# Kernel optimization log

Hardware: AMD Instinct MI355X
Metric: run time of the kernel (lower is better)

The kernel has to match this reference:

```python
import jax, jax.numpy as jnp
import numpy as np

EMBED_DIM = 1024
NUM_HEADS = 16
HEAD_DIM = EMBED_DIM // NUM_HEADS
NEG_INF = -1e9


def setup_inputs() -> dict:
    key = jax.random.key(0)
    k1, k2, k3, k4, k5 = jax.random.split(key, 5)
    # ragged batch: 8 segments, alternating lengths 1024 / 512 -> 6144 tokens
    lengths = np.array([1024, 512, 1024, 512, 1024, 512, 1024, 512], dtype=np.int32)
    cu_seqlens = np.concatenate([[0], np.cumsum(lengths)]).astype(np.int32)
    total = int(cu_seqlens[-1])  # 6144
    scale = 0.02
    return {
        "hidden_states": jax.random.normal(k1, (total, EMBED_DIM), dtype=jnp.float32),
        "proj_weight": jax.random.normal(k2, (3 * EMBED_DIM, EMBED_DIM), dtype=jnp.float32) * scale,
        "proj_bias": jax.random.normal(k3, (3 * EMBED_DIM,), dtype=jnp.float32) * scale,
        "out_weight": jax.random.normal(k4, (EMBED_DIM, EMBED_DIM), dtype=jnp.float32) * scale,
        "out_bias": jax.random.normal(k5, (EMBED_DIM,), dtype=jnp.float32) * scale,
        "cu_seqlens": jnp.asarray(cu_seqlens),
        "max_len": 1024,
    }


def reference(hidden_states, proj_weight, proj_bias, out_weight, out_bias, cu_seqlens, max_len):
    T = hidden_states.shape[0]
    B = cu_seqlens.shape[0] - 1
    H, Dh = NUM_HEADS, HEAD_DIM
    softmax_scale = 1.0 / jnp.sqrt(jnp.float32(Dh))

    # fused QKV projection: [T, 3E] -> [T, H, 3, Dh]
    qkv = hidden_states @ proj_weight.T + proj_bias
    qkv = qkv.reshape(T, H, 3, Dh)
    q, k, v = qkv[:, :, 0], qkv[:, :, 1], qkv[:, :, 2]  # each [T, H, Dh]

    # unpack ragged tokens into padded [B, S, H, Dh]
    lengths = cu_seqlens[1:] - cu_seqlens[:-1]            # [B]
    pos = jnp.arange(max_len)                              # [S]
    valid = pos[None, :] < lengths[:, None]                # [B, S]
    idx = jnp.where(valid, cu_seqlens[:-1, None] + pos[None, :], 0)  # [B, S]
    qp, kp, vp = q[idx], k[idx], v[idx]                    # [B, S, H, Dh]

    # per-segment attention (non-causal encoder self-attn)
    scores = jnp.einsum("bqhd,bkhd->bhqk", qp, kp) * softmax_scale  # [B,H,S,S]
    scores = jnp.where(valid[:, None, None, :], scores, NEG_INF)
    probs = jax.nn.softmax(scores, axis=-1)
    ctx = jnp.einsum("bhqk,bkhd->bqhd", probs, vp)         # [B, S, H, Dh]

    # pack back to ragged [T, E]; invalid slots scattered out-of-bounds (dropped)
    scatter_idx = jnp.where(valid, idx, T).reshape(-1)     # [B*S]
    ctx_flat = ctx.reshape(B * max_len, H * Dh)
    context = jnp.zeros((T, H * Dh), dtype=ctx_flat.dtype).at[scatter_idx].set(
        ctx_flat, mode="drop")

    return context @ out_weight.T + out_bias
```

## Files before the change

kernel.cpp:

```cpp
#include <hip/hip_runtime.h>
#include <math.h>

#define EMBED 1024
#define NHEAD 16
#define HDIM 64
#define QKV_LD 3072
#define SM_SCALE_LOG2 0.18033688f

typedef _Float16 f16x8 __attribute__((ext_vector_type(8)));
typedef float f32x4 __attribute__((ext_vector_type(4)));
typedef unsigned short ushort8v __attribute__((ext_vector_type(8)));
typedef unsigned short ushort4v __attribute__((ext_vector_type(4)));

__device__ __forceinline__ void gload16(const void* g, void* l) {
    __builtin_amdgcn_global_load_lds(
        (const __attribute__((address_space(1))) unsigned int*)g,
        (__attribute__((address_space(3))) unsigned int*)l, 16, 0, 0);
}

__device__ __forceinline__ int xcd_swz(int bid, int nwg) {
    int cpx = nwg >> 3;
    return (bid & 7) * cpx + (bid >> 3);
}

__device__ __forceinline__ int swz(int row, int col) {
    return row * 72 + (col ^ (((row >> 3) & 7) << 3));
}

__global__ __launch_bounds__(256) void cvt3_f32_f16(
    const float* __restrict__ xa, _Float16* __restrict__ ya, int nA,
    const float* __restrict__ xb, _Float16* __restrict__ yb, int nB,
    const float* __restrict__ xc, _Float16* __restrict__ yc, int nC)
{
    int i = blockIdx.x * 256 + threadIdx.x;
    const float* x;
    _Float16* y;
    if (i < nA)               { x = xa; y = ya; }
    else if (i < nA + nB)     { x = xb; y = yb; i -= nA; }
    else if (i < nA + nB + nC){ x = xc; y = yc; i -= nA + nB; }
    else return;
    float4 v = reinterpret_cast<const float4*>(x)[i];
    unsigned short h0 = __builtin_bit_cast(unsigned short, (_Float16)v.x);
    unsigned short h1 = __builtin_bit_cast(unsigned short, (_Float16)v.y);
    unsigned short h2 = __builtin_bit_cast(unsigned short, (_Float16)v.z);
    unsigned short h3 = __builtin_bit_cast(unsigned short, (_Float16)v.w);
    reinterpret_cast<ushort4*>(y)[i] = make_ushort4(h0, h1, h2, h3);
}

template <bool F16_OUT>
__global__ __launch_bounds__(256) void gemm_m97(
    const _Float16* __restrict__ A, const _Float16* __restrict__ B,
    const float* __restrict__ bias, float* __restrict__ Cf,
    _Float16* __restrict__ Ch, int M, int N, int K, int gx)
{
    __shared__ __align__(16) unsigned short sA[128 * 64];
    __shared__ __align__(16) unsigned short sB[128 * 64];

    const int nwg = gridDim.x;
    const int wgid = xcd_swz(blockIdx.x, nwg);
    const int row0 = (wgid / gx) * 128;
    const int col0 = (wgid % gx) * 128;

    const int tid = threadIdx.x;
    const int lane = tid & 63;
    const int w = tid >> 6;
    const int wr = w >> 1;
    const int wc = w & 1;
    const int c = lane & 15;
    const int g = lane >> 4;

    const unsigned short* Au = (const unsigned short*)A;
    const unsigned short* Bu = (const unsigned short*)B;

    f32x4 acc[4][4];
    #pragma unroll
    for (int m = 0; m < 4; m++)
        #pragma unroll
        for (int n = 0; n < 4; n++)
            acc[m][n] = (f32x4){0.f, 0.f, 0.f, 0.f};

    size_t aoff[4], boff[4];
    int ldst[4];
    #pragma unroll
    for (int i = 0; i < 4; i++) {
        int chunk = (i * 4 + w) * 64 + lane;
        int row = chunk >> 3;
        int scol = ((chunk & 7) ^ (row & 7)) * 8;
        aoff[i] = (size_t)min(row0 + row, M - 1) * K + scol;
        boff[i] = (size_t)min(col0 + row, N - 1) * K + scol;
        ldst[i] = chunk * 8;
    }

    for (int k0 = 0; k0 < K; k0 += 64) {
        __syncthreads();
        #pragma unroll
        for (int i = 0; i < 4; i++) {
            gload16(Au + aoff[i] + k0, &sA[ldst[i]]);
            gload16(Bu + boff[i] + k0, &sB[ldst[i]]);
        }
        __syncthreads();

        #pragma unroll
        for (int ks = 0; ks < 2; ks++) {
            f16x8 af[4], bf[4];
            #pragma unroll
            for (int m = 0; m < 4; m++) {
                int row = wr * 64 + m * 16 + c;
                int cc = (ks * 4 + g) ^ (row & 7);
                af[m] = __builtin_bit_cast(f16x8, *reinterpret_cast<const ushort8v*>(
                            &sA[row * 64 + cc * 8]));
            }
            #pragma unroll
            for (int n = 0; n < 4; n++) {
                int row = wc * 64 + n * 16 + c;
                int cc = (ks * 4 + g) ^ (row & 7);
                bf[n] = __builtin_bit_cast(f16x8, *reinterpret_cast<const ushort8v*>(
                            &sB[row * 64 + cc * 8]));
            }
            #pragma unroll
            for (int m = 0; m < 4; m++)
                #pragma unroll
                for (int n = 0; n < 4; n++)
                    acc[m][n] = __builtin_amdgcn_mfma_f32_16x16x32_f16(af[m], bf[n], acc[m][n], 0, 0, 0);
        }
    }

    #pragma unroll
    for (int m = 0; m < 4; m++) {
        #pragma unroll
        for (int n = 0; n < 4; n++) {
            int cc = col0 + wc * 64 + n * 16 + c;
            if (cc >= N) continue;
            float bv = bias[cc];
            #pragma unroll
            for (int j = 0; j < 4; j++) {
                int r = row0 + wr * 64 + m * 16 + g * 4 + j;
                if (r >= M) continue;
                float v = acc[m][n][j] + bv;
                if constexpr (F16_OUT) {
                    Ch[(size_t)r * N + cc] = (_Float16)v;
                } else {
                    Cf[(size_t)r * N + cc] = v;
                }
            }
        }
    }
}

__global__ __launch_bounds__(256) void attn_mfma(
    const _Float16* __restrict__ qkv, const int* __restrict__ cu,
    _Float16* __restrict__ ctx, int B, int maxTiles)
{
    __shared__ __align__(16) unsigned short sK[64 * 72];
    __shared__ __align__(16) unsigned short sV[64 * 72];

    const int nwg = gridDim.x;
    const int wgid = xcd_swz(blockIdx.x, nwg);
    const int h = wgid / maxTiles;
    const int tile = wgid % maxTiles;

    int b = -1, q0 = 0, accum = 0;
    for (int i = 0; i < B; i++) {
        int len = cu[i + 1] - cu[i];
        int nt = (len + 63) >> 6;
        if (tile < accum + nt) { b = i; q0 = (tile - accum) << 6; break; }
        accum += nt;
    }
    if (b < 0) return;
    const int s0 = cu[b];
    const int L = cu[b + 1] - s0;
    if (q0 >= L) return;

    const int tid = threadIdx.x;
    const int lane = tid & 63;
    const int w = tid >> 6;
    const int g = lane >> 4;
    const int c = lane & 15;
    const size_t qcol = (size_t)h * 192;
    const unsigned short* qkvu = (const unsigned short*)qkv;

    f16x8 q[2];
    {
        int qrow = min(q0 + w * 16 + c, L - 1);
        size_t off = (size_t)(s0 + qrow) * QKV_LD + qcol + g * 8;
        q[0] = *reinterpret_cast<const f16x8*>(&qkv[off]);
        q[1] = *reinterpret_cast<const f16x8*>(&qkv[off + 32]);
    }

    f32x4 o[4];
    #pragma unroll
    for (int n = 0; n < 4; n++) o[n] = (f32x4){0.f, 0.f, 0.f, 0.f};
    float m_r = -INFINITY;
    float l_r = 0.f;

    for (int kc = 0; kc < L; kc += 64) {
        __syncthreads();
        #pragma unroll
        for (int it = 0; it < 2; it++) {
            int idx = it * 256 + tid;
            int r = idx >> 3;
            int d0 = (idx & 7) * 8;
            int gr = min(kc + r, L - 1);
            size_t off = (size_t)(s0 + gr) * QKV_LD + qcol + 64 + d0;
            *reinterpret_cast<uint4*>(&sK[swz(r, d0)]) =
                *reinterpret_cast<const uint4*>(&qkvu[off]);
            ushort8v vv = *reinterpret_cast<const ushort8v*>(&qkvu[off + 64]);
            #pragma unroll
            for (int j = 0; j < 8; j++)
                sV[swz(d0 + j, r)] = vv[j];
        }
        __syncthreads();

        __builtin_amdgcn_s_setprio(1);
        f32x4 sacc[4];
        #pragma unroll
        for (int f = 0; f < 4; f++) sacc[f] = (f32x4){0.f, 0.f, 0.f, 0.f};
        #pragma unroll
        for (int f = 0; f < 4; f++) {
            #pragma unroll
            for (int ks = 0; ks < 2; ks++) {
                f16x8 kf = __builtin_bit_cast(f16x8, *reinterpret_cast<const ushort8v*>(
                               &sK[swz(f * 16 + c, ks * 32 + g * 8)]));
                sacc[f] = __builtin_amdgcn_mfma_f32_16x16x32_f16(kf, q[ks], sacc[f], 0, 0, 0);
            }
        }
        __builtin_amdgcn_s_setprio(0);

        float mx = -INFINITY;
        if (kc + 64 <= L) {
            #pragma unroll
            for (int f = 0; f < 4; f++) {
                #pragma unroll
                for (int j = 0; j < 4; j++) {
                    float v = sacc[f][j] * SM_SCALE_LOG2;
                    sacc[f][j] = v;
                    mx = fmaxf(mx, v);
                }
            }
        } else {
            #pragma unroll
            for (int f = 0; f < 4; f++) {
                #pragma unroll
                for (int j = 0; j < 4; j++) {
                    float v = sacc[f][j] * SM_SCALE_LOG2;
                    if (kc + f * 16 + g * 4 + j >= L) v = -1.0e9f;
                    sacc[f][j] = v;
                    mx = fmaxf(mx, v);
                }
            }
        }
        mx = fmaxf(mx, __shfl_xor(mx, 16));
        mx = fmaxf(mx, __shfl_xor(mx, 32));

        const bool nskip = !__all(mx - m_r <= 8.0f);
        const float mn = nskip ? fmaxf(m_r, mx) : m_r;

        unsigned int paw[4][2];
        float rs = 0.f;
        #pragma unroll
        for (int f = 0; f < 4; f++) {
            float p0 = exp2f(sacc[f][0] - mn);
            float p1 = exp2f(sacc[f][1] - mn);
            float p2 = exp2f(sacc[f][2] - mn);
            float p3 = exp2f(sacc[f][3] - mn);
            rs += (p0 + p1) + (p2 + p3);
            unsigned int h0 = __builtin_bit_cast(unsigned short, (_Float16)p0);
            unsigned int h1 = __builtin_bit_cast(unsigned short, (_Float16)p1);
            unsigned int h2 = __builtin_bit_cast(unsigned short, (_Float16)p2);
            unsigned int h3 = __builtin_bit_cast(unsigned short, (_Float16)p3);
            paw[f][0] = h0 | (h1 << 16);
            paw[f][1] = h2 | (h3 << 16);
        }
        rs += __shfl_xor(rs, 16);
        rs += __shfl_xor(rs, 32);

        if (nskip) {
            float fs = exp2f(m_r - mn);
            l_r = l_r * fs + rs;
            m_r = mn;
            #pragma unroll
            for (int j = 0; j < 4; j++) {
                float fq = __shfl(fs, (lane & 48) | (g * 4 + j));
                #pragma unroll
                for (int n = 0; n < 4; n++)
                    o[n][j] *= fq;
            }
        } else {
            l_r += rs;
        }

        __builtin_amdgcn_s_setprio(1);
        #pragma unroll
        for (int ks = 0; ks < 2; ks++) {
            uint4 pw;
            pw.x = paw[2 * ks][0];
            pw.y = paw[2 * ks][1];
            pw.z = paw[2 * ks + 1][0];
            pw.w = paw[2 * ks + 1][1];
            f16x8 pa = __builtin_bit_cast(f16x8, pw);
            #pragma unroll
            for (int n = 0; n < 4; n++) {
                uint2 lo = *reinterpret_cast<const uint2*>(
                               &sV[swz(n * 16 + c, ks * 32 + g * 4)]);
                uint2 hi = *reinterpret_cast<const uint2*>(
                               &sV[swz(n * 16 + c, ks * 32 + 16 + g * 4)]);
                uint4 vw;
                vw.x = lo.x; vw.y = lo.y; vw.z = hi.x; vw.w = hi.y;
                f16x8 vf = __builtin_bit_cast(f16x8, vw);
                o[n] = __builtin_amdgcn_mfma_f32_16x16x32_f16(pa, vf, o[n], 0, 0, 0);
            }
        }
        __builtin_amdgcn_s_setprio(0);
    }

    float linv[4];
    {
        float il = 1.0f / l_r;
        #pragma unroll
        for (int j = 0; j < 4; j++)
            linv[j] = __shfl(il, (lane & 48) | (g * 4 + j));
    }
    #pragma unroll
    for (int n = 0; n < 4; n++) {
        #pragma unroll
        for (int j = 0; j < 4; j++) {
            int r = q0 + w * 16 + g * 4 + j;
            if (r >= L) continue;
            ctx[(size_t)(s0 + r) * EMBED + h * HDIM + n * 16 + c] =
                (_Float16)(o[n][j] * linv[j]);
        }
    }
}

extern "C" void kernel_launch(void* const* d_in, const int* in_sizes, int n_in,
                              void* d_out, int out_size, void* d_ws, size_t ws_size,
                              hipStream_t stream) {
    const float* hs = (const float*)d_in[0];
    const float* pw = (const float*)d_in[1];
    const float* pb = (const float*)d_in[2];
    const float* ow = (const float*)d_in[3];
    const float* ob = (const float*)d_in[4];
    const int*   cu = (const int*)d_in[5];

    const int T = in_sizes[0] / EMBED;
    const int B = in_sizes[5] - 1;

    char* p = (char*)d_ws;
    size_t hsF_b  = (size_t)T * EMBED * sizeof(_Float16);
    size_t pwF_b  = (size_t)3 * EMBED * EMBED * sizeof(_Float16);
    size_t owF_b  = (size_t)EMBED * EMBED * sizeof(_Float16);
    size_t qkvF_b = (size_t)T * QKV_LD * sizeof(_Float16);
    size_t ctxF_b = hsF_b;

    _Float16* hsF  = (_Float16*)p;  p += hsF_b;
    _Float16* pwF  = (_Float16*)p;  p += pwF_b;
    _Float16* owF  = (_Float16*)p;  p += owF_b;
    _Float16* qkvF = (_Float16*)p;  p += qkvF_b;
    _Float16* ctxF = (_Float16*)p;  p += ctxF_b;

    float* out = (float*)d_out;
    dim3 blk(256);

    {
        int nA = T * EMBED / 4;
        int nB = 3 * EMBED * EMBED / 4;
        int nC = EMBED * EMBED / 4;
        int total = nA + nB + nC;
        cvt3_f32_f16<<<(total + 255) / 256, blk, 0, stream>>>(
            hs, hsF, nA, pw, pwF, nB, ow, owF, nC);
    }

    {
        int gx = (3 * EMBED) / 128;
        int nwg = gx * ((T + 127) / 128);
        gemm_m97<true><<<nwg, blk, 0, stream>>>(hsF, pwF, pb,
                                                (float*)nullptr, qkvF,
                                                T, 3 * EMBED, EMBED, gx);
    }

    {
        int maxTiles = T / 64 + B;
        int nwg = NHEAD * maxTiles;
        attn_mfma<<<nwg, blk, 0, stream>>>(qkvF, cu, ctxF, B, maxTiles);
    }

    {
        int gx = EMBED / 128;
        int nwg = gx * ((T + 127) / 128);
        gemm_m97<false><<<nwg, blk, 0, stream>>>(ctxF, owF, ob,
                                                 out, (_Float16*)nullptr,
                                                 T, EMBED, EMBED, gx);
    }
}
```

Measured before the change: 174.1 us.

## Load K fragments directly from global and register-prefetch next V tile

Drops the shared-memory staging buffer for K. Each wave now reads its own K MFMA fragments straight from global memory into registers. The V tile for the next iteration is prefetched into registers while the current one is consumed, so its global latency overlaps the compute. The aim is to cut LDS traffic and to hide V load latency. In exchange, each of the four waves reloads the same K rows from global or L2 (four times the K reads), and register pressure goes up.

Result: slower. 217.9 us (+25.2%).

```diff
diff --git a/kernel.cpp b/kernel.cpp
--- a/kernel.cpp
+++ b/kernel.cpp
@@ -151,7 +151,6 @@
     const _Float16* __restrict__ qkv, const int* __restrict__ cu,
     _Float16* __restrict__ ctx, int B, int maxTiles)
 {
-    __shared__ __align__(16) unsigned short sK[64 * 72];
     __shared__ __align__(16) unsigned short sV[64 * 72];
 
     const int nwg = gridDim.x;
@@ -187,6 +186,19 @@
         q[1] = *reinterpret_cast<const f16x8*>(&qkv[off + 32]);
     }
 
+    const int r0_ = tid >> 3;
+    const int r1_ = 32 + r0_;
+    const int d0_ = (tid & 7) * 8;
+    const size_t vband = qcol + 128 + d0_;
+
+    ushort8v vv0, vv1;
+    {
+        int gr0 = min(r0_, L - 1);
+        int gr1 = min(r1_, L - 1);
+        vv0 = *reinterpret_cast<const ushort8v*>(&qkvu[(size_t)(s0 + gr0) * QKV_LD + vband]);
+        vv1 = *reinterpret_cast<const ushort8v*>(&qkvu[(size_t)(s0 + gr1) * QKV_LD + vband]);
+    }
+
     f32x4 o[4];
     #pragma unroll
     for (int n = 0; n < 4; n++) o[n] = (f32x4){0.f, 0.f, 0.f, 0.f};
@@ -194,20 +206,29 @@
     float l_r = 0.f;
 
     for (int kc = 0; kc < L; kc += 64) {
+        f16x8 kf[4][2];
+        #pragma unroll
+        for (int f = 0; f < 4; f++) {
+            int kr = min(kc + f * 16 + c, L - 1);
+            size_t koff = (size_t)(s0 + kr) * QKV_LD + qcol + 64 + g * 8;
+            kf[f][0] = *reinterpret_cast<const f16x8*>(&qkv[koff]);
+            kf[f][1] = *reinterpret_cast<const f16x8*>(&qkv[koff + 32]);
+        }
+
         __syncthreads();
         #pragma unroll
-        for (int it = 0; it < 2; it++) {
-            int idx = it * 256 + tid;
-            int r = idx >> 3;
-            int d0 = (idx & 7) * 8;
-            int gr = min(kc + r, L - 1);
-            size_t off = (size_t)(s0 + gr) * QKV_LD + qcol + 64 + d0;
-            *reinterpret_cast<uint4*>(&sK[swz(r, d0)]) =
-                *reinterpret_cast<const uint4*>(&qkvu[off]);
-            ushort8v vv = *reinterpret_cast<const ushort8v*>(&qkvu[off + 64]);
-            #pragma unroll
-            for (int j = 0; j < 8; j++)
-                sV[swz(d0 + j, r)] = vv[j];
+        for (int j = 0; j < 8; j++)
+            sV[swz(d0_ + j, r0_)] = vv0[j];
+        #pragma unroll
+        for (int j = 0; j < 8; j++)
+            sV[swz(d0_ + j, r1_)] = vv1[j];
+
+        if (kc + 64 < L) {
+            int nkc = kc + 64;
+            int gr0 = min(nkc + r0_, L - 1);
+            int gr1 = min(nkc + r1_, L - 1);
+            vv0 = *reinterpret_cast<const ushort8v*>(&qkvu[(size_t)(s0 + gr0) * QKV_LD + vband]);
+            vv1 = *reinterpret_cast<const ushort8v*>(&qkvu[(size_t)(s0 + gr1) * QKV_LD + vband]);
         }
         __syncthreads();
 
@@ -218,11 +239,8 @@
         #pragma unroll
         for (int f = 0; f < 4; f++) {
             #pragma unroll
-            for (int ks = 0; ks < 2; ks++) {
-                f16x8 kf = __builtin_bit_cast(f16x8, *reinterpret_cast<const ushort8v*>(
-                               &sK[swz(f * 16 + c, ks * 32 + g * 8)]));
-                sacc[f] = __builtin_amdgcn_mfma_f32_16x16x32_f16(kf, q[ks], sacc[f], 0, 0, 0);
-            }
+            for (int ks = 0; ks < 2; ks++)
+                sacc[f] = __builtin_amdgcn_mfma_f32_16x16x32_f16(kf[f][ks], q[ks], sacc[f], 0, 0, 0);
         }
         __builtin_amdgcn_s_setprio(0);
 
```

## Double-buffer K/V tiles in attention with register prefetch of next chunk

Applied to the files above, without the earlier changes.

The attention kernel now keeps two LDS buffers for K and V. The next 64-row chunk is loaded from global memory into registers before the current chunk's QK and PV MFMAs, then written to the alternate buffer afterwards. This hides global load latency behind compute and cuts the barriers per iteration from two to one. In exchange it doubles LDS use and raises register pressure, which can lower occupancy.

Result: slower. 178.6 us (+2.6%).

```diff
diff --git a/kernel.cpp b/kernel.cpp
--- a/kernel.cpp
+++ b/kernel.cpp
@@ -151,8 +151,8 @@
     const _Float16* __restrict__ qkv, const int* __restrict__ cu,
     _Float16* __restrict__ ctx, int B, int maxTiles)
 {
-    __shared__ __align__(16) unsigned short sK[64 * 72];
-    __shared__ __align__(16) unsigned short sV[64 * 72];
+    __shared__ __align__(16) unsigned short sK[2][64 * 72];
+    __shared__ __align__(16) unsigned short sV[2][64 * 72];
 
     const int nwg = gridDim.x;
     const int wgid = xcd_swz(blockIdx.x, nwg);
@@ -187,6 +187,34 @@
         q[1] = *reinterpret_cast<const f16x8*>(&qkv[off + 32]);
     }
 
+    const int r0_ = tid >> 3;
+    const int r1_ = 32 + r0_;
+    const int d0_ = (tid & 7) * 8;
+    const int lk0 = swz(r0_, d0_);
+    const int lk1 = swz(r1_, d0_);
+    const size_t kband = qcol + 64 + d0_;
+    const size_t vband = qcol + 128 + d0_;
+
+    uint4 kr0, kr1;
+    ushort8v vv0, vv1;
+
+    {
+        int g0 = min(r0_, L - 1);
+        int g1 = min(r1_, L - 1);
+        kr0 = *reinterpret_cast<const uint4*>(&qkvu[(size_t)(s0 + g0) * QKV_LD + kband]);
+        kr1 = *reinterpret_cast<const uint4*>(&qkvu[(size_t)(s0 + g1) * QKV_LD + kband]);
+        vv0 = *reinterpret_cast<const ushort8v*>(&qkvu[(size_t)(s0 + g0) * QKV_LD + vband]);
+        vv1 = *reinterpret_cast<const ushort8v*>(&qkvu[(size_t)(s0 + g1) * QKV_LD + vband]);
+        *reinterpret_cast<uint4*>(&sK[0][lk0]) = kr0;
+        *reinterpret_cast<uint4*>(&sK[0][lk1]) = kr1;
+        #pragma unroll
+        for (int j = 0; j < 8; j++) {
+            sV[0][swz(d0_ + j, r0_)] = vv0[j];
+            sV[0][swz(d0_ + j, r1_)] = vv1[j];
+        }
+    }
+    __syncthreads();
+
     f32x4 o[4];
     #pragma unroll
     for (int n = 0; n < 4; n++) o[n] = (f32x4){0.f, 0.f, 0.f, 0.f};
@@ -194,22 +222,18 @@
     float l_r = 0.f;
 
     for (int kc = 0; kc < L; kc += 64) {
-        __syncthreads();
-        #pragma unroll
-        for (int it = 0; it < 2; it++) {
-            int idx = it * 256 + tid;
-            int r = idx >> 3;
-            int d0 = (idx & 7) * 8;
-            int gr = min(kc + r, L - 1);
-            size_t off = (size_t)(s0 + gr) * QKV_LD + qcol + 64 + d0;
-            *reinterpret_cast<uint4*>(&sK[swz(r, d0)]) =
-                *reinterpret_cast<const uint4*>(&qkvu[off]);
-            ushort8v vv = *reinterpret_cast<const ushort8v*>(&qkvu[off + 64]);
-            #pragma unroll
-            for (int j = 0; j < 8; j++)
-                sV[swz(d0 + j, r)] = vv[j];
-        }
-        __syncthreads();
+        const int p = (kc >> 6) & 1;
+        const bool more = (kc + 64 < L);
+
+        if (more) {
+            int nk = kc + 64;
+            int g0 = min(nk + r0_, L - 1);
+            int g1 = min(nk + r1_, L - 1);
+            kr0 = *reinterpret_cast<const uint4*>(&qkvu[(size_t)(s0 + g0) * QKV_LD + kband]);
+            kr1 = *reinterpret_cast<const uint4*>(&qkvu[(size_t)(s0 + g1) * QKV_LD + kband]);
+            vv0 = *reinterpret_cast<const ushort8v*>(&qkvu[(size_t)(s0 + g0) * QKV_LD + vband]);
+            vv1 = *reinterpret_cast<const ushort8v*>(&qkvu[(size_t)(s0 + g1) * QKV_LD + vband]);
+        }
 
         __builtin_amdgcn_s_setprio(1);
         f32x4 sacc[4];
@@ -220,7 +244,7 @@
             #pragma unroll
             for (int ks = 0; ks < 2; ks++) {
                 f16x8 kf = __builtin_bit_cast(f16x8, *reinterpret_cast<const ushort8v*>(
-                               &sK[swz(f * 16 + c, ks * 32 + g * 8)]));
+                               &sK[p][swz(f * 16 + c, ks * 32 + g * 8)]));
                 sacc[f] = __builtin_amdgcn_mfma_f32_16x16x32_f16(kf, q[ks], sacc[f], 0, 0, 0);
             }
         }
@@ -301,9 +325,9 @@
             #pragma unroll
             for (int n = 0; n < 4; n++) {
                 uint2 lo = *reinterpret_cast<const uint2*>(
-                               &sV[swz(n * 16 + c, ks * 32 + g * 4)]);
+                               &sV[p][swz(n * 16 + c, ks * 32 + g * 4)]);
                 uint2 hi = *reinterpret_cast<const uint2*>(
-                               &sV[swz(n * 16 + c, ks * 32 + 16 + g * 4)]);
+                               &sV[p][swz(n * 16 + c, ks * 32 + 16 + g * 4)]);
                 uint4 vw;
                 vw.x = lo.x; vw.y = lo.y; vw.z = hi.x; vw.w = hi.y;
                 f16x8 vf = __builtin_bit_cast(f16x8, vw);
@@ -311,6 +335,17 @@
             }
         }
         __builtin_amdgcn_s_setprio(0);
+
+        if (more) {
+            *reinterpret_cast<uint4*>(&sK[1 - p][lk0]) = kr0;
+            *reinterpret_cast<uint4*>(&sK[1 - p][lk1]) = kr1;
+            #pragma unroll
+            for (int j = 0; j < 8; j++) {
+                sV[1 - p][swz(d0_ + j, r0_)] = vv0[j];
+                sV[1 - p][swz(d0_ + j, r1_)] = vv1[j];
+            }
+        }
+        __syncthreads();
     }
 
     float linv[4];
```
